# Kernel tuning notes

Hardware: AMD Instinct MI355X
Metric: run time of the kernel (lower is better)

Reference implementation:

```python
import jax, jax.numpy as jnp
import numpy as np

B, S, H, W = 64, 32, 40, 64
SENS, UNITS, MOTOR, NA = 1283, 48, 4, 2
UNFOLDS = 6  # ncps LTC default ode_unfolds
EPS = 1e-8


def setup_inputs() -> dict:
    key = jax.random.key(0)
    ks = iter(jax.random.split(key, 40))
    u = lambda sh, lo, hi: jax.random.uniform(next(ks), sh, jnp.float32, lo, hi)
    inp = {}
    inp["depth_image"] = jax.random.uniform(next(ks), (B, S, H, W), jnp.float32)
    inp["relative_position"] = jax.random.normal(next(ks), (B, S, 3), jnp.float32)
    # CNN params (conv k3 s2 p1 + ReLU) x3: 1->32->64->32
    def cw(o, i):
        return jax.random.normal(next(ks), (o, i, 3, 3), jnp.float32) / np.sqrt(i * 9.0)
    inp["w1"], inp["b1"] = cw(32, 1), jnp.zeros((32,), jnp.float32)
    inp["w2"], inp["b2"] = cw(64, 32), jnp.zeros((64,), jnp.float32)
    inp["w3"], inp["b3"] = cw(32, 64), jnp.zeros((32,), jnp.float32)
    # LTC cell params (ncps init ranges)
    inp["input_w"] = jnp.ones((SENS,), jnp.float32)
    inp["input_b"] = jnp.zeros((SENS,), jnp.float32)
    inp["sens_w"] = u((SENS, UNITS), 0.001, 1.0)
    inp["sens_mu"] = u((SENS, UNITS), 0.3, 0.8)
    inp["sens_sigma"] = u((SENS, UNITS), 3.0, 8.0)
    inp["sens_erev"] = jnp.sign(jax.random.normal(next(ks), (SENS, UNITS)))
    inp["rec_w"] = u((UNITS, UNITS), 0.001, 1.0)
    inp["rec_mu"] = u((UNITS, UNITS), 0.3, 0.8)
    inp["rec_sigma"] = u((UNITS, UNITS), 3.0, 8.0)
    inp["rec_erev"] = jnp.sign(jax.random.normal(next(ks), (UNITS, UNITS)))
    inp["gleak"] = u((UNITS,), 0.001, 1.0)
    inp["vleak"] = u((UNITS,), -0.2, 0.2)
    inp["cm"] = u((UNITS,), 0.4, 0.6)
    inp["out_w"] = jnp.ones((MOTOR,), jnp.float32)
    inp["out_b"] = jnp.zeros((MOTOR,), jnp.float32)
    inp["head_w"] = jax.random.normal(next(ks), (MOTOR, NA), jnp.float32) * 0.5
    inp["head_b"] = jnp.zeros((NA,), jnp.float32)
    inp["sens_mask"] = (jax.random.uniform(next(ks), (SENS, UNITS)) < 0.3).astype(jnp.int32)
    inp["rec_mask"] = (jax.random.uniform(next(ks), (UNITS, UNITS)) < 0.3).astype(jnp.int32)
    return inp


def _conv(x, w, b):
    y = jax.lax.conv_general_dilated(x, w, (2, 2), [(1, 1), (1, 1)],
                                     dimension_numbers=("NCHW", "OIHW", "NCHW"))
    return jax.nn.relu(y + b[None, :, None, None])


def reference(depth_image, relative_position, w1, b1, w2, b2, w3, b3,
              input_w, input_b, sens_w, sens_mu, sens_sigma, sens_erev,
              rec_w, rec_mu, rec_sigma, rec_erev, gleak, vleak, cm,
              out_w, out_b, head_w, head_b, sens_mask, rec_mask):
    b, s = depth_image.shape[:2]
    x = depth_image.reshape(b * s, 1, H, W)
    x = _conv(_conv(_conv(x, w1, b1), w2, b2), w3, b3)  # [b*s,32,5,8]
    feat = x.reshape(b, s, -1)  # [b,s,1280]
    seq = jnp.concatenate([feat, relative_position.reshape(b, s, -1)], axis=2)  # [b,s,1283]

    sp = jax.nn.softplus
    smask = sens_mask.astype(seq.dtype)
    rmask = rec_mask.astype(seq.dtype)
    cm_t = sp(cm) * UNFOLDS          # cm / (elapsed_time / ode_unfolds), dt=1
    gl = sp(gleak)
    sw_pos = sp(sens_w) * smask
    rw_pos = sp(rec_w) * rmask

    def step(v, xt):  # xt: [b, SENS]
        I = xt * input_w + input_b
        # sensory synapse activations: [b, SENS, UNITS]
        sa = sw_pos * jax.nn.sigmoid(sens_sigma * (I[:, :, None] - sens_mu))
        w_num_s = (sa * sens_erev).sum(1)  # [b, UNITS]
        w_den_s = sa.sum(1)
        def unfold(v, _):
            ra = rw_pos * jax.nn.sigmoid(rec_sigma * (v[:, :, None] - rec_mu))
            num = cm_t * v + gl * vleak + (ra * rec_erev).sum(1) + w_num_s
            den = cm_t + gl + ra.sum(1) + w_den_s
            return num / (den + EPS), None
        v, _ = jax.lax.scan(unfold, v, None, length=UNFOLDS)
        y = v[:, :MOTOR] * out_w + out_b  # motor neuron readout
        return v, y

    v0 = jnp.zeros((b, UNITS), seq.dtype)
    _, ys = jax.lax.scan(step, v0, jnp.swapaxes(seq, 0, 1))  # [s, b, MOTOR]
    pooled = ys.mean(0)  # mean over seq dim
    return jnp.tanh(pooled @ head_w + head_b)  # [b, NA] action mean
```

## Files before the change

### kernel.cpp

```cpp
#include <hip/hip_runtime.h>
#include <hip/hip_bf16.h>


typedef __attribute__((ext_vector_type(8))) short bshort8;
typedef __attribute__((ext_vector_type(4))) float f32x4;

constexpr long OFF_SEQ  = 0;
constexpr long OFF_SP4  = 2627584;
constexpr long OFF_RP4  = 2873920;
constexpr long OFF_CM   = 2886208;
constexpr long OFF_W2B  = 2886400;
constexpr long OFF_W3B  = 2898688;
constexpr long OFF_PART = 2907904;

__device__ __forceinline__ float sp_(float x) {
    return fmaxf(x, 0.f) + log1pf(expf(-fabsf(x)));
}

__device__ __forceinline__ float qxor1_(float x) {
    return __int_as_float(__builtin_amdgcn_mov_dpp(__float_as_int(x), 0xB1, 0xF, 0xF, true));
}
__device__ __forceinline__ float qxor2_(float x) {
    return __int_as_float(__builtin_amdgcn_mov_dpp(__float_as_int(x), 0x4E, 0xF, 0xF, true));
}

__global__ void prep_kernel(const float* __restrict__ sens_w, const float* __restrict__ sens_mu,
                            const float* __restrict__ sens_sigma, const float* __restrict__ sens_erev,
                            const int* __restrict__ sens_mask,
                            const float* __restrict__ rec_w, const float* __restrict__ rec_mu,
                            const float* __restrict__ rec_sigma, const float* __restrict__ rec_erev,
                            const int* __restrict__ rec_mask,
                            const float* __restrict__ gleak, const float* __restrict__ vleak,
                            const float* __restrict__ cm,
                            const float* __restrict__ w2, const float* __restrict__ w3,
                            float* __restrict__ ws) {
    const float L2E = 1.4426950408889634f;
    int i = blockIdx.x * 256 + threadIdx.x;
    if (i < 61584) {
        float m  = sens_mask[i] ? 1.f : 0.f;
        float sw = sp_(sens_w[i]) * m;
        float sg = sens_sigma[i], mu = sens_mu[i];
        ((float4*)(ws + OFF_SP4))[i] =
            make_float4(-sg * L2E, sg * mu * L2E, sw * sens_erev[i], sw);
    } else if (i < 64656) {
        int q = i - 61584;
        int j = q >> 6, u = q & 63;
        float4 v = make_float4(0.f, 0.f, 0.f, 0.f);
        if (u < 48) {
            int idx = j * 48 + u;
            float m  = rec_mask[idx] ? 1.f : 0.f;
            float sw = sp_(rec_w[idx]) * m;
            float sg = rec_sigma[idx], mu = rec_mu[idx];
            v = make_float4(-sg * L2E, sg * mu * L2E, sw * rec_erev[idx], sw);
        }
        ((float4*)(ws + OFF_RP4))[q] = v;
    } else if (i < 64704) {
        int u = i - 64656;
        float g = sp_(gleak[u]);
        ws[OFF_CM + u]       = sp_(cm[u]) * 6.f;
        ws[OFF_CM + 64 + u]  = g;
        ws[OFF_CM + 128 + u] = g * vleak[u];
    } else if (i < 89280) {
        int n = i - 64704;
        int j = n & 7, l = (n >> 3) & 63, t2 = n >> 9;
        int wv = t2 & 3;
        int r  = t2 >> 2;
        int xp = r & 1, hk = r >> 1;
        int ky = hk % 3, h = hk / 3;
        int oc = wv * 16 + (l & 15);
        int kgB = l >> 4;
        int icl = (kgB & 1) * 8 + j;
        int ic = h * 16 + icl;
        int kx = 2 * xp + (kgB >> 1);
        float val = (kx == 3) ? 0.f : w2[((oc * 32 + ic) * 3 + ky) * 3 + kx];
        ((__hip_bfloat16*)(ws + OFF_W2B))[n] = __float2bfloat16(val);
    } else if (i < 107712) {
        int n = i - 89280;
        int j = n & 7, l = (n >> 3) & 63, t3 = n >> 9;
        int h = t3 & 1, u2 = t3 >> 1;
        int nt = u2 / 9, p = u2 % 9;
        int ky = p / 3, kx = p % 3;
        int oc = nt * 16 + (l & 15);
        int ic = h * 32 + (l >> 4) * 8 + j;
        ((__hip_bfloat16*)(ws + OFF_W3B))[n] =
            __float2bfloat16(w3[((oc * 64 + ic) * 3 + ky) * 3 + kx]);
    }
}

#define IMGB 0
#define C1H  5424
#define A2E  0
#define A2O  12672
#define SMB  28272

__global__ __launch_bounds__(256, 4) void cnn_kernel(
    const float* __restrict__ depth, const float* __restrict__ relpos,
    const float* __restrict__ w1, const float* __restrict__ b1,
    const float* __restrict__ b2, const float* __restrict__ b3,
    const __hip_bfloat16* __restrict__ w2b, const __hip_bfloat16* __restrict__ w3b,
    float* __restrict__ seq) {
    __shared__ __align__(16) char smraw[SMB];
    const int t = threadIdx.x;
    const int img = blockIdx.x;
    const int l = t & 63;
    const int wvu = __builtin_amdgcn_readfirstlane(t >> 6);
    const int m = l & 15, kg = l >> 4;

    for (int i = t; i < 7068; i += 256) ((uint*)smraw)[i] = 0u;
    __syncthreads();
    for (int i = t; i < 1280; i += 256) {
        int pos = 2 * i;
        int h = pos >> 6, w = pos & 63;
        float2 d = *(const float2*)(depth + (long)img * 2560 + pos);
        __hip_bfloat162 pk = __float22bfloat162_rn(d);
        *(__hip_bfloat162*)(smraw + IMGB + ((h + 1) * 66 + (w + 2)) * 2) = pk;
    }
    __syncthreads();

    const __hip_bfloat16* imgp = (const __hip_bfloat16*)(smraw + IMGB);
    f32x4 acc[10];
    {
        float bias = b2[wvu * 16 + m];
#pragma unroll
        for (int mt = 0; mt < 10; ++mt) acc[mt] = (f32x4){bias, bias, bias, bias};
    }

#pragma unroll 1
    for (int h = 0; h < 2; ++h) {
        const int ocb = h * 16 + wvu * 4;
        float wv4[4][9], bv4[4];
#pragma unroll
        for (int j = 0; j < 4; ++j) {
            bv4[j] = b1[ocb + j];
#pragma unroll
            for (int k = 0; k < 9; ++k) wv4[j][k] = w1[(ocb + j) * 9 + k];
        }
#pragma unroll 1
        for (int i = 0; i < 10; ++i) {
            int p = l + (i << 6);
            int y1 = p >> 5, x1 = p & 31;
            float xin[9];
#pragma unroll
            for (int ky = 0; ky < 3; ++ky)
#pragma unroll
                for (int kx = 0; kx < 3; ++kx)
                    xin[ky * 3 + kx] = __bfloat162float(imgp[(2 * y1 + ky) * 66 + 2 * x1 + kx + 1]);
            float o[4];
#pragma unroll
            for (int j = 0; j < 4; ++j) {
                float a = bv4[j];
#pragma unroll
                for (int k = 0; k < 9; ++k) a = fmaf(wv4[j][k], xin[k], a);
                o[j] = fmaxf(a, 0.f);
            }
            char* cb = smraw + C1H + (((y1 + 1) * 34) + (x1 + 1)) * 32 + wvu * 8;
            *(__hip_bfloat162*)cb       = __float22bfloat162_rn(make_float2(o[0], o[1]));
            *(__hip_bfloat162*)(cb + 4) = __float22bfloat162_rn(make_float2(o[2], o[3]));
        }
        bshort8 Bh[6];
#pragma unroll
        for (int f = 0; f < 6; ++f)
            Bh[f] = *(const bshort8*)(w2b + (((h * 6 + f) * 4 + wvu) * 64 + l) * 8);
        __syncthreads();
#pragma unroll
        for (int ky = 0; ky < 3; ++ky) {
#pragma unroll
            for (int xp = 0; xp < 2; ++xp) {
                bshort8 Bp = Bh[ky * 2 + xp];
                const char* base = smraw + C1H + (ky * 34 + 2 * m + 2 * xp + (kg >> 1)) * 32 + (kg & 1) * 16;
#pragma unroll
                for (int mt = 0; mt < 10; ++mt) {
                    bshort8 A = *(const bshort8*)(base + mt * 2176);
                    acc[mt] = __builtin_amdgcn_mfma_f32_16x16x32_bf16(A, Bp, acc[mt], 0, 0, 0);
                }
            }
        }
        __syncthreads();
    }

    for (int i = t; i < 6336; i += 256) ((uint*)smraw)[i] = 0u;
    __syncthreads();
    {
        int oc = wvu * 16 + m;
        int q = oc >> 3, sub = oc & 7;
#pragma unroll
        for (int mt = 0; mt < 10; ++mt) {
            int row = mt + 1;
#pragma unroll
            for (int reg = 0; reg < 4; ++reg) {
                int x2 = kg * 4 + reg;
                int odd = x2 & 1;
                int xi = odd ? ((x2 + 1) >> 1) : (x2 >> 1);
                char* ab = smraw + (odd ? A2O : A2E);
                float v = fmaxf(acc[mt][reg], 0.f);
                *(__hip_bfloat16*)(ab + (((q * 11 + row) * 9 + xi) * 8 + sub) * 2) = __float2bfloat16(v);
            }
        }
    }
    __syncthreads();

    {
        const int nt = wvu & 1;
        const bool two = wvu < 2;
        f32x4 c3a = (f32x4){0.f, 0.f, 0.f, 0.f};
        f32x4 c3b = (f32x4){0.f, 0.f, 0.f, 0.f};
        const int xb = m & 7, yb = m >> 3;
#pragma unroll
        for (int p = 0; p < 9; ++p) {
            int ky = p / 3, kx = p % 3;
            const char* arr = smraw + ((kx == 1) ? A2E : A2O);
            int xi3 = xb + (kx == 2);
#pragma unroll
            for (int h = 0; h < 2; ++h) {
                bshort8 B = *(const bshort8*)(w3b + (((nt * 9 + p) * 2 + h) * 64 + l) * 8);
                int q = h * 4 + kg;
                const char* base = arr + ((q * 11 + 2 * yb + ky) * 9 + xi3) * 16;
                if (two) {
                    bshort8 A0 = *(const bshort8*)(base);
                    c3a = __builtin_amdgcn_mfma_f32_16x16x32_bf16(A0, B, c3a, 0, 0, 0);
                    bshort8 A2 = *(const bshort8*)(base + 1152);
                    c3b = __builtin_amdgcn_mfma_f32_16x16x32_bf16(A2, B, c3b, 0, 0, 0);
                } else {
                    bshort8 A1 = *(const bshort8*)(base + 576);
                    c3a = __builtin_amdgcn_mfma_f32_16x16x32_bf16(A1, B, c3a, 0, 0, 0);
                }
            }
        }
        __syncthreads();
        float* sb = (float*)smraw;
        int oc = nt * 16 + m;
        float bv = b3[oc];
        int ob40 = oc * 40;
        if (two) {
#pragma unroll
            for (int reg = 0; reg < 4; ++reg) {
                sb[ob40 + kg * 4 + reg] = fmaxf(c3a[reg] + bv, 0.f);
                int px2 = 32 + kg * 4 + reg;
                if (px2 < 40) sb[ob40 + px2] = fmaxf(c3b[reg] + bv, 0.f);
            }
        } else {
#pragma unroll
            for (int reg = 0; reg < 4; ++reg)
                sb[ob40 + 16 + kg * 4 + reg] = fmaxf(c3a[reg] + bv, 0.f);
        }
        __syncthreads();
        for (int i = t; i < 1283; i += 256)
            seq[(long)img * 1283 + i] = (i < 1280) ? sb[i] : relpos[img * 3 + (i - 1280)];
    }
}

__global__ __launch_bounds__(768) void sensory_kernel(
    const float* __restrict__ sp, const float* __restrict__ seq,
    const float* __restrict__ iw, const float* __restrict__ ibias,
    float2* __restrict__ part) {
    const float4* P4 = (const float4*)sp;
    __shared__ __align__(16) char sbuf[49152];
    float*  IT  = (float*)sbuf;
    float2* red = (float2*)sbuf;
    const int t = threadIdx.x;
    const int pb = blockIdx.x * 8;

    for (int p = 0; p < 8; ++p)
        for (int k = t; k < 1283; k += 768)
            IT[k * 8 + p] = fmaf(seq[(long)(pb + p) * 1283 + k], iw[k], ibias[k]);
    __syncthreads();

    const int u = t % 48, kg = t / 48;
    float2 acc[8];
#pragma unroll
    for (int p = 0; p < 8; ++p) acc[p] = make_float2(0.f, 0.f);

#pragma unroll 2
    for (int i = 0; i < 81; ++i) {
        int k = kg + 16 * i;
        if (k < 1283) {
            float4 pv = P4[k * 48 + u];
            float4 Ia = *(const float4*)&IT[k * 8];
            float4 Ib = *(const float4*)&IT[k * 8 + 4];
            float r0 = __builtin_amdgcn_rcpf(1.f + __builtin_amdgcn_exp2f(fmaf(pv.x, Ia.x, pv.y)));
            float r1 = __builtin_amdgcn_rcpf(1.f + __builtin_amdgcn_exp2f(fmaf(pv.x, Ia.y, pv.y)));
            float r2 = __builtin_amdgcn_rcpf(1.f + __builtin_amdgcn_exp2f(fmaf(pv.x, Ia.z, pv.y)));
            float r3 = __builtin_amdgcn_rcpf(1.f + __builtin_amdgcn_exp2f(fmaf(pv.x, Ia.w, pv.y)));
            float r4 = __builtin_amdgcn_rcpf(1.f + __builtin_amdgcn_exp2f(fmaf(pv.x, Ib.x, pv.y)));
            float r5 = __builtin_amdgcn_rcpf(1.f + __builtin_amdgcn_exp2f(fmaf(pv.x, Ib.y, pv.y)));
            float r6 = __builtin_amdgcn_rcpf(1.f + __builtin_amdgcn_exp2f(fmaf(pv.x, Ib.z, pv.y)));
            float r7 = __builtin_amdgcn_rcpf(1.f + __builtin_amdgcn_exp2f(fmaf(pv.x, Ib.w, pv.y)));
            acc[0].x = fmaf(pv.z, r0, acc[0].x); acc[0].y = fmaf(pv.w, r0, acc[0].y);
            acc[1].x = fmaf(pv.z, r1, acc[1].x); acc[1].y = fmaf(pv.w, r1, acc[1].y);
            acc[2].x = fmaf(pv.z, r2, acc[2].x); acc[2].y = fmaf(pv.w, r2, acc[2].y);
            acc[3].x = fmaf(pv.z, r3, acc[3].x); acc[3].y = fmaf(pv.w, r3, acc[3].y);
            acc[4].x = fmaf(pv.z, r4, acc[4].x); acc[4].y = fmaf(pv.w, r4, acc[4].y);
            acc[5].x = fmaf(pv.z, r5, acc[5].x); acc[5].y = fmaf(pv.w, r5, acc[5].y);
            acc[6].x = fmaf(pv.z, r6, acc[6].x); acc[6].y = fmaf(pv.w, r6, acc[6].y);
            acc[7].x = fmaf(pv.z, r7, acc[7].x); acc[7].y = fmaf(pv.w, r7, acc[7].y);
        }
    }
    __syncthreads();
#pragma unroll
    for (int p = 0; p < 8; ++p) red[(kg * 8 + p) * 48 + u] = acc[p];
    __syncthreads();
    if (t < 384) {
        int p = t / 48, uu = t - p * 48;
        float sn = 0.f, sd = 0.f;
#pragma unroll
        for (int g = 0; g < 16; ++g) {
            float2 rr = red[(g * 8 + p) * 48 + uu];
            sn += rr.x; sd += rr.y;
        }
        part[(long)(pb + p) * 48 + uu] = make_float2(sn, sd);
    }
}

__global__ __launch_bounds__(192, 1) void recurrent_kernel(
    const float* __restrict__ rp, const float* __restrict__ cmglv,
    const float2* __restrict__ part,
    const float* __restrict__ out_w, const float* __restrict__ out_b,
    const float* __restrict__ head_w, const float* __restrict__ head_b,
    float* __restrict__ outp) {
    __shared__ float2 WL[1536];
    __shared__ float  LV[2][64];
    __shared__ float  ym[4];
    const int t  = threadIdx.x;
    const int b  = blockIdx.x;
    const int u  = t >> 2;
    const int jq = t & 3;

    const float4* RP4 = (const float4*)rp;
    float4 P[12];
#pragma unroll
    for (int r = 0; r < 12; ++r) P[r] = RP4[(jq * 12 + r) * 64 + u];
#pragma unroll
    for (int r = 0; r < 12; ++r) {
        asm volatile("" : "+v"(P[r].x), "+v"(P[r].y), "+v"(P[r].z), "+v"(P[r].w));
    }

    for (int i = t; i < 1536; i += 192) WL[i] = part[(long)b * 1536 + i];
    if (t < 64) { LV[0][t] = 0.f; LV[1][t] = 0.f; }

    const float cmt = cmglv[u], gl = cmglv[64 + u], glv = cmglv[128 + u];
    const float cg  = cmt + gl + 1e-8f;
    float ow = 0.f, ob = 0.f;
    const bool lead = (jq == 0) && (u < 4);
    if (lead) { ow = out_w[u]; ob = out_b[u]; }
    __syncthreads();

    float vn = 0.f, yacc = 0.f;
    int buf = 0;
#pragma unroll 1
    for (int s = 0; s < 32; ++s) {
        float2 wnd = WL[s * 48 + u];
        const float basen = glv + wnd.x;
        const float based = cg + wnd.y;
#pragma unroll
        for (int unf = 0; unf < 6; ++unf) {
            const float4* lv4 = (const float4*)&LV[buf][jq * 12];
            float4 V0 = lv4[0], V1 = lv4[1], V2 = lv4[2];
            float va[12] = {V0.x, V0.y, V0.z, V0.w, V1.x, V1.y, V1.z, V1.w,
                            V2.x, V2.y, V2.z, V2.w};
            float pn = 0.f, pd = 0.f;
#pragma unroll
            for (int r = 0; r < 12; ++r) {
                float rr = __builtin_amdgcn_rcpf(
                    1.f + __builtin_amdgcn_exp2f(fmaf(P[r].x, va[r], P[r].y)));
                pn = fmaf(P[r].z, rr, pn);
                pd = fmaf(P[r].w, rr, pd);
            }
            pn += qxor1_(pn); pd += qxor1_(pd);
            pn += qxor2_(pn); pd += qxor2_(pd);
            float num = fmaf(cmt, vn, basen) + pn;
            float den = based + pd;
            float r0 = __builtin_amdgcn_rcpf(den);
            r0 = r0 * fmaf(-den, r0, 2.f);
            vn = num * r0;
            if (jq == 0) LV[buf ^ 1][u] = vn;
            __syncthreads();
            buf ^= 1;
        }
        if (lead) yacc = fmaf(vn, ow, yacc) + ob;
    }
    if (lead) ym[u] = yacc;
    __syncthreads();
    if (t < 2) {
        const float inv = 1.f / 32.f;
        float o = fmaf(ym[0] * inv, head_w[t],
                  fmaf(ym[1] * inv, head_w[2 + t],
                  fmaf(ym[2] * inv, head_w[4 + t],
                  fmaf(ym[3] * inv, head_w[6 + t], head_b[t]))));
        outp[b * 2 + t] = tanhf(o);
    }
}

extern "C" void kernel_launch(void* const* d_in, const int* in_sizes, int n_in,
                              void* d_out, int out_size, void* d_ws, size_t ws_size,
                              hipStream_t stream) {
    const float* depth      = (const float*)d_in[0];
    const float* relpos     = (const float*)d_in[1];
    const float* w1         = (const float*)d_in[2];
    const float* b1         = (const float*)d_in[3];
    const float* w2         = (const float*)d_in[4];
    const float* b2         = (const float*)d_in[5];
    const float* w3         = (const float*)d_in[6];
    const float* b3         = (const float*)d_in[7];
    const float* iw         = (const float*)d_in[8];
    const float* ibias      = (const float*)d_in[9];
    const float* sens_w     = (const float*)d_in[10];
    const float* sens_mu    = (const float*)d_in[11];
    const float* sens_sigma = (const float*)d_in[12];
    const float* sens_erev  = (const float*)d_in[13];
    const float* rec_w      = (const float*)d_in[14];
    const float* rec_mu     = (const float*)d_in[15];
    const float* rec_sigma  = (const float*)d_in[16];
    const float* rec_erev   = (const float*)d_in[17];
    const float* gleak      = (const float*)d_in[18];
    const float* vleak      = (const float*)d_in[19];
    const float* cm         = (const float*)d_in[20];
    const float* out_w      = (const float*)d_in[21];
    const float* out_b      = (const float*)d_in[22];
    const float* head_w     = (const float*)d_in[23];
    const float* head_b     = (const float*)d_in[24];
    const int*   sens_mask  = (const int*)d_in[25];
    const int*   rec_mask   = (const int*)d_in[26];

    float* ws  = (float*)d_ws;
    float* out = (float*)d_out;

    prep_kernel<<<477, 256, 0, stream>>>(sens_w, sens_mu, sens_sigma, sens_erev, sens_mask,
                                         rec_w, rec_mu, rec_sigma, rec_erev, rec_mask,
                                         gleak, vleak, cm, w2, w3, ws);
    cnn_kernel<<<2048, 256, 0, stream>>>(depth, relpos, w1, b1, b2, b3,
                                         (const __hip_bfloat16*)(ws + OFF_W2B),
                                         (const __hip_bfloat16*)(ws + OFF_W3B),
                                         ws + OFF_SEQ);
    sensory_kernel<<<256, 768, 0, stream>>>(ws + OFF_SP4, ws + OFF_SEQ, iw, ibias,
                                            (float2*)(ws + OFF_PART));
    recurrent_kernel<<<64, 192, 0, stream>>>(ws + OFF_RP4, ws + OFF_CM,
                                             (const float2*)(ws + OFF_PART),
                                             out_w, out_b, head_w, head_b, out);
}
```

Baseline: 274.7 us.

## Process two batch elements per block in recurrent kernel

Each recurrent block now advances two independent batch sequences together, interleaving their sigmoid and reduction chains so the two dependency chains can hide each other's latency, and shares the barriers between them. The grid is halved from 64 to 32 blocks. The cost is fewer blocks on a GPU with many idle compute units, and more registers and LDS per block.

Measured after the change: 311.1 us. 13.2% more time.

```diff
diff --git a/kernel.cpp b/kernel.cpp
--- a/kernel.cpp
+++ b/kernel.cpp
@@ -317,11 +317,11 @@
     const float* __restrict__ out_w, const float* __restrict__ out_b,
     const float* __restrict__ head_w, const float* __restrict__ head_b,
     float* __restrict__ outp) {
-    __shared__ float2 WL[1536];
-    __shared__ float  LV[2][64];
-    __shared__ float  ym[4];
+    __shared__ float2 WL[2][1536];
+    __shared__ float  LV[2][2][64];
+    __shared__ float  ym[2][4];
     const int t  = threadIdx.x;
-    const int b  = blockIdx.x;
+    const int bA = blockIdx.x * 2;
     const int u  = t >> 2;
     const int jq = t & 3;
 
@@ -334,8 +334,11 @@
         asm volatile("" : "+v"(P[r].x), "+v"(P[r].y), "+v"(P[r].z), "+v"(P[r].w));
     }
 
-    for (int i = t; i < 1536; i += 192) WL[i] = part[(long)b * 1536 + i];
-    if (t < 64) { LV[0][t] = 0.f; LV[1][t] = 0.f; }
+    for (int i = t; i < 3072; i += 192) {
+        int lb = i / 1536, li = i - lb * 1536;
+        WL[lb][li] = part[(long)(bA + lb) * 1536 + li];
+    }
+    if (t < 64) { LV[0][0][t] = 0.f; LV[0][1][t] = 0.f; LV[1][0][t] = 0.f; LV[1][1][t] = 0.f; }
 
     const float cmt = cmglv[u], gl = cmglv[64 + u], glv = cmglv[128 + u];
     const float cg  = cmt + gl + 1e-8f;
@@ -344,49 +347,64 @@
     if (lead) { ow = out_w[u]; ob = out_b[u]; }
     __syncthreads();
 
-    float vn = 0.f, yacc = 0.f;
+    float vnA = 0.f, vnB = 0.f, yaccA = 0.f, yaccB = 0.f;
     int buf = 0;
 #pragma unroll 1
     for (int s = 0; s < 32; ++s) {
-        float2 wnd = WL[s * 48 + u];
-        const float basen = glv + wnd.x;
-        const float based = cg + wnd.y;
+        float2 wA = WL[0][s * 48 + u];
+        float2 wB = WL[1][s * 48 + u];
+        const float basenA = glv + wA.x, basedA = cg + wA.y;
+        const float basenB = glv + wB.x, basedB = cg + wB.y;
 #pragma unroll
         for (int unf = 0; unf < 6; ++unf) {
-            const float4* lv4 = (const float4*)&LV[buf][jq * 12];
-            float4 V0 = lv4[0], V1 = lv4[1], V2 = lv4[2];
-            float va[12] = {V0.x, V0.y, V0.z, V0.w, V1.x, V1.y, V1.z, V1.w,
-                            V2.x, V2.y, V2.z, V2.w};
-            float pn = 0.f, pd = 0.f;
+            const float4* lvA = (const float4*)&LV[0][buf][jq * 12];
+            const float4* lvB = (const float4*)&LV[1][buf][jq * 12];
+            float4 A0 = lvA[0], A1 = lvA[1], A2 = lvA[2];
+            float4 B0 = lvB[0], B1 = lvB[1], B2 = lvB[2];
+            float vaA[12] = {A0.x, A0.y, A0.z, A0.w, A1.x, A1.y, A1.z, A1.w,
+                             A2.x, A2.y, A2.z, A2.w};
+            float vaB[12] = {B0.x, B0.y, B0.z, B0.w, B1.x, B1.y, B1.z, B1.w,
+                             B2.x, B2.y, B2.z, B2.w};
+            float pnA = 0.f, pdA = 0.f, pnB = 0.f, pdB = 0.f;
 #pragma unroll
             for (int r = 0; r < 12; ++r) {
-                float rr = __builtin_amdgcn_rcpf(
-                    1.f + __builtin_amdgcn_exp2f(fmaf(P[r].x, va[r], P[r].y)));
-                pn = fmaf(P[r].z, rr, pn);
-                pd = fmaf(P[r].w, rr, pd);
-            }
-            pn += qxor1_(pn); pd += qxor1_(pd);
-            pn += qxor2_(pn); pd += qxor2_(pd);
-            float num = fmaf(cmt, vn, basen) + pn;
-            float den = based + pd;
-            float r0 = __builtin_amdgcn_rcpf(den);
-            r0 = r0 * fmaf(-den, r0, 2.f);
-            vn = num * r0;
-            if (jq == 0) LV[buf ^ 1][u] = vn;
+                float rA = __builtin_amdgcn_rcpf(
+                    1.f + __builtin_amdgcn_exp2f(fmaf(P[r].x, vaA[r], P[r].y)));
+                float rB = __builtin_amdgcn_rcpf(
+                    1.f + __builtin_amdgcn_exp2f(fmaf(P[r].x, vaB[r], P[r].y)));
+                pnA = fmaf(P[r].z, rA, pnA); pdA = fmaf(P[r].w, rA, pdA);
+                pnB = fmaf(P[r].z, rB, pnB); pdB = fmaf(P[r].w, rB, pdB);
+            }
+            pnA += qxor1_(pnA); pdA += qxor1_(pdA);
+            pnB += qxor1_(pnB); pdB += qxor1_(pdB);
+            pnA += qxor2_(pnA); pdA += qxor2_(pdA);
+            pnB += qxor2_(pnB); pdB += qxor2_(pdB);
+            float numA = fmaf(cmt, vnA, basenA) + pnA;
+            float denA = basedA + pdA;
+            float numB = fmaf(cmt, vnB, basenB) + pnB;
+            float denB = basedB + pdB;
+            float rA0 = __builtin_amdgcn_rcpf(denA);
+            rA0 = rA0 * fmaf(-denA, rA0, 2.f);
+            float rB0 = __builtin_amdgcn_rcpf(denB);
+            rB0 = rB0 * fmaf(-denB, rB0, 2.f);
+            vnA = numA * rA0;
+            vnB = numB * rB0;
+            if (jq == 0) { LV[0][buf ^ 1][u] = vnA; LV[1][buf ^ 1][u] = vnB; }
             __syncthreads();
             buf ^= 1;
         }
-        if (lead) yacc = fmaf(vn, ow, yacc) + ob;
-    }
-    if (lead) ym[u] = yacc;
-    __syncthreads();
-    if (t < 2) {
+        if (lead) { yaccA = fmaf(vnA, ow, yaccA) + ob; yaccB = fmaf(vnB, ow, yaccB) + ob; }
+    }
+    if (lead) { ym[0][u] = yaccA; ym[1][u] = yaccB; }
+    __syncthreads();
+    if (t < 4) {
+        int lb = t >> 1, g = t & 1;
         const float inv = 1.f / 32.f;
-        float o = fmaf(ym[0] * inv, head_w[t],
-                  fmaf(ym[1] * inv, head_w[2 + t],
-                  fmaf(ym[2] * inv, head_w[4 + t],
-                  fmaf(ym[3] * inv, head_w[6 + t], head_b[t]))));
-        outp[b * 2 + t] = tanhf(o);
+        float o = fmaf(ym[lb][0] * inv, head_w[g],
+                  fmaf(ym[lb][1] * inv, head_w[2 + g],
+                  fmaf(ym[lb][2] * inv, head_w[4 + g],
+                  fmaf(ym[lb][3] * inv, head_w[6 + g], head_b[g]))));
+        outp[(bA + lb) * 2 + g] = tanhf(o);
     }
 }
 
@@ -433,7 +451,7 @@
                                          ws + OFF_SEQ);
     sensory_kernel<<<256, 768, 0, stream>>>(ws + OFF_SP4, ws + OFF_SEQ, iw, ibias,
                                             (float2*)(ws + OFF_PART));
-    recurrent_kernel<<<64, 192, 0, stream>>>(ws + OFF_RP4, ws + OFF_CM,
+    recurrent_kernel<<<32, 192, 0, stream>>>(ws + OFF_RP4, ws + OFF_CM,
                                              (const float2*)(ws + OFF_PART),
                                              out_w, out_b, head_w, head_b, out);
 }
```

## Compact sparse sensory synapses per unit and iterate only over masked entries

Applied to the files above, without the earlier changes.

A new kernel builds, for each of the 48 units, a compacted list of the sensory synapses whose mask is set. It stores the precomputed parameters and source indices, capped at 480 entries and zero-padded. The sensory kernel now loops over 30 compacted entries per thread group instead of all 1283 inputs, cutting the exp/rcp work that previously ran on masked-out synapses. The input activations are transposed in shared memory so they can be gathered by index, which may cause LDS bank conflicts. The fixed capacity silently drops synapses if a unit ever has more than 480 connections.

Result: faster. 261.4 us (-4.9%).

```diff
diff --git a/kernel.cpp b/kernel.cpp
--- a/kernel.cpp
+++ b/kernel.cpp
@@ -13,6 +13,8 @@
 constexpr long OFF_W3B  = 2898688;
 constexpr long OFF_PART = 2907904;
 
+constexpr int SCAP = 480;
+
 __device__ __forceinline__ float sp_(float x) {
     return fmaxf(x, 0.f) + log1pf(expf(-fabsf(x)));
 }
@@ -24,10 +26,7 @@
     return __int_as_float(__builtin_amdgcn_mov_dpp(__float_as_int(x), 0x4E, 0xF, 0xF, true));
 }
 
-__global__ void prep_kernel(const float* __restrict__ sens_w, const float* __restrict__ sens_mu,
-                            const float* __restrict__ sens_sigma, const float* __restrict__ sens_erev,
-                            const int* __restrict__ sens_mask,
-                            const float* __restrict__ rec_w, const float* __restrict__ rec_mu,
+__global__ void prep_kernel(const float* __restrict__ rec_w, const float* __restrict__ rec_mu,
                             const float* __restrict__ rec_sigma, const float* __restrict__ rec_erev,
                             const int* __restrict__ rec_mask,
                             const float* __restrict__ gleak, const float* __restrict__ vleak,
@@ -35,14 +34,8 @@
                             const float* __restrict__ w2, const float* __restrict__ w3,
                             float* __restrict__ ws) {
     const float L2E = 1.4426950408889634f;
-    int i = blockIdx.x * 256 + threadIdx.x;
-    if (i < 61584) {
-        float m  = sens_mask[i] ? 1.f : 0.f;
-        float sw = sp_(sens_w[i]) * m;
-        float sg = sens_sigma[i], mu = sens_mu[i];
-        ((float4*)(ws + OFF_SP4))[i] =
-            make_float4(-sg * L2E, sg * mu * L2E, sw * sens_erev[i], sw);
-    } else if (i < 64656) {
+    int i = blockIdx.x * 256 + threadIdx.x + 61584;
+    if (i < 64656) {
         int q = i - 61584;
         int j = q >> 6, u = q & 63;
         float4 v = make_float4(0.f, 0.f, 0.f, 0.f);
@@ -87,6 +80,54 @@
     }
 }
 
+__global__ __launch_bounds__(256) void sens_compact_kernel(
+    const float* __restrict__ sens_w, const float* __restrict__ sens_mu,
+    const float* __restrict__ sens_sigma, const float* __restrict__ sens_erev,
+    const int* __restrict__ sens_mask, float* __restrict__ ws) {
+    const float L2E = 1.4426950408889634f;
+    float4* cp4 = (float4*)(ws + OFF_SP4);
+    int* kix = (int*)(ws + OFF_SP4 + 98304);
+    int* nnz = (int*)(ws + OFF_SP4 + 122880);
+    const int u = blockIdx.x;
+    const int t = threadIdx.x;
+    const int w = t >> 6, lane = t & 63;
+    __shared__ int wcnt[4];
+    __shared__ int basetot;
+    if (t == 0) basetot = 0;
+    __syncthreads();
+#pragma unroll 1
+    for (int c = 0; c < 6; ++c) {
+        int k = c * 256 + t;
+        bool m = (k < 1283) && (sens_mask[k * 48 + u] != 0);
+        unsigned long long bal = __ballot(m);
+        int prefix = __popcll(bal & ((1ULL << lane) - 1ULL));
+        if (lane == 0) wcnt[w] = __popcll(bal);
+        __syncthreads();
+        int wbase = basetot;
+        for (int ww = 0; ww < 4; ++ww) if (ww < w) wbase += wcnt[ww];
+        if (m) {
+            int pos = wbase + prefix;
+            if (pos < SCAP) {
+                int idx = k * 48 + u;
+                float sw = sp_(sens_w[idx]);
+                float sg = sens_sigma[idx], mu = sens_mu[idx];
+                cp4[pos * 48 + u] = make_float4(-sg * L2E, sg * mu * L2E,
+                                                sw * sens_erev[idx], sw);
+                kix[pos * 48 + u] = k;
+            }
+        }
+        __syncthreads();
+        if (t == 0) basetot += wcnt[0] + wcnt[1] + wcnt[2] + wcnt[3];
+        __syncthreads();
+    }
+    int cnt = min(basetot, SCAP);
+    for (int e = cnt + t; e < SCAP; e += 256) {
+        cp4[e * 48 + u] = make_float4(0.f, 0.f, 0.f, 0.f);
+        kix[e * 48 + u] = 0;
+    }
+    if (t == 0) nnz[u] = cnt;
+}
+
 #define IMGB 0
 #define C1H  5424
 #define A2E  0
@@ -253,7 +294,8 @@
     const float* __restrict__ sp, const float* __restrict__ seq,
     const float* __restrict__ iw, const float* __restrict__ ibias,
     float2* __restrict__ part) {
-    const float4* P4 = (const float4*)sp;
+    const float4* CP4 = (const float4*)sp;
+    const int* KIX = (const int*)(sp + 98304);
     __shared__ __align__(16) char sbuf[49152];
     float*  IT  = (float*)sbuf;
     float2* red = (float2*)sbuf;
@@ -262,7 +304,7 @@
 
     for (int p = 0; p < 8; ++p)
         for (int k = t; k < 1283; k += 768)
-            IT[k * 8 + p] = fmaf(seq[(long)(pb + p) * 1283 + k], iw[k], ibias[k]);
+            IT[p * 1288 + k] = fmaf(seq[(long)(pb + p) * 1283 + k], iw[k], ibias[k]);
     __syncthreads();
 
     const int u = t % 48, kg = t / 48;
@@ -271,29 +313,27 @@
     for (int p = 0; p < 8; ++p) acc[p] = make_float2(0.f, 0.f);
 
 #pragma unroll 2
-    for (int i = 0; i < 81; ++i) {
-        int k = kg + 16 * i;
-        if (k < 1283) {
-            float4 pv = P4[k * 48 + u];
-            float4 Ia = *(const float4*)&IT[k * 8];
-            float4 Ib = *(const float4*)&IT[k * 8 + 4];
-            float r0 = __builtin_amdgcn_rcpf(1.f + __builtin_amdgcn_exp2f(fmaf(pv.x, Ia.x, pv.y)));
-            float r1 = __builtin_amdgcn_rcpf(1.f + __builtin_amdgcn_exp2f(fmaf(pv.x, Ia.y, pv.y)));
-            float r2 = __builtin_amdgcn_rcpf(1.f + __builtin_amdgcn_exp2f(fmaf(pv.x, Ia.z, pv.y)));
-            float r3 = __builtin_amdgcn_rcpf(1.f + __builtin_amdgcn_exp2f(fmaf(pv.x, Ia.w, pv.y)));
-            float r4 = __builtin_amdgcn_rcpf(1.f + __builtin_amdgcn_exp2f(fmaf(pv.x, Ib.x, pv.y)));
-            float r5 = __builtin_amdgcn_rcpf(1.f + __builtin_amdgcn_exp2f(fmaf(pv.x, Ib.y, pv.y)));
-            float r6 = __builtin_amdgcn_rcpf(1.f + __builtin_amdgcn_exp2f(fmaf(pv.x, Ib.z, pv.y)));
-            float r7 = __builtin_amdgcn_rcpf(1.f + __builtin_amdgcn_exp2f(fmaf(pv.x, Ib.w, pv.y)));
-            acc[0].x = fmaf(pv.z, r0, acc[0].x); acc[0].y = fmaf(pv.w, r0, acc[0].y);
-            acc[1].x = fmaf(pv.z, r1, acc[1].x); acc[1].y = fmaf(pv.w, r1, acc[1].y);
-            acc[2].x = fmaf(pv.z, r2, acc[2].x); acc[2].y = fmaf(pv.w, r2, acc[2].y);
-            acc[3].x = fmaf(pv.z, r3, acc[3].x); acc[3].y = fmaf(pv.w, r3, acc[3].y);
-            acc[4].x = fmaf(pv.z, r4, acc[4].x); acc[4].y = fmaf(pv.w, r4, acc[4].y);
-            acc[5].x = fmaf(pv.z, r5, acc[5].x); acc[5].y = fmaf(pv.w, r5, acc[5].y);
-            acc[6].x = fmaf(pv.z, r6, acc[6].x); acc[6].y = fmaf(pv.w, r6, acc[6].y);
-            acc[7].x = fmaf(pv.z, r7, acc[7].x); acc[7].y = fmaf(pv.w, r7, acc[7].y);
-        }
+    for (int i = 0; i < 30; ++i) {
+        int e = kg + 16 * i;
+        float4 pv = CP4[e * 48 + u];
+        int k = KIX[e * 48 + u];
+        const float* itk = IT + k;
+        float r0 = __builtin_amdgcn_rcpf(1.f + __builtin_amdgcn_exp2f(fmaf(pv.x, itk[0 * 1288], pv.y)));
+        float r1 = __builtin_amdgcn_rcpf(1.f + __builtin_amdgcn_exp2f(fmaf(pv.x, itk[1 * 1288], pv.y)));
+        float r2 = __builtin_amdgcn_rcpf(1.f + __builtin_amdgcn_exp2f(fmaf(pv.x, itk[2 * 1288], pv.y)));
+        float r3 = __builtin_amdgcn_rcpf(1.f + __builtin_amdgcn_exp2f(fmaf(pv.x, itk[3 * 1288], pv.y)));
+        float r4 = __builtin_amdgcn_rcpf(1.f + __builtin_amdgcn_exp2f(fmaf(pv.x, itk[4 * 1288], pv.y)));
+        float r5 = __builtin_amdgcn_rcpf(1.f + __builtin_amdgcn_exp2f(fmaf(pv.x, itk[5 * 1288], pv.y)));
+        float r6 = __builtin_amdgcn_rcpf(1.f + __builtin_amdgcn_exp2f(fmaf(pv.x, itk[6 * 1288], pv.y)));
+        float r7 = __builtin_amdgcn_rcpf(1.f + __builtin_amdgcn_exp2f(fmaf(pv.x, itk[7 * 1288], pv.y)));
+        acc[0].x = fmaf(pv.z, r0, acc[0].x); acc[0].y = fmaf(pv.w, r0, acc[0].y);
+        acc[1].x = fmaf(pv.z, r1, acc[1].x); acc[1].y = fmaf(pv.w, r1, acc[1].y);
+        acc[2].x = fmaf(pv.z, r2, acc[2].x); acc[2].y = fmaf(pv.w, r2, acc[2].y);
+        acc[3].x = fmaf(pv.z, r3, acc[3].x); acc[3].y = fmaf(pv.w, r3, acc[3].y);
+        acc[4].x = fmaf(pv.z, r4, acc[4].x); acc[4].y = fmaf(pv.w, r4, acc[4].y);
+        acc[5].x = fmaf(pv.z, r5, acc[5].x); acc[5].y = fmaf(pv.w, r5, acc[5].y);
+        acc[6].x = fmaf(pv.z, r6, acc[6].x); acc[6].y = fmaf(pv.w, r6, acc[6].y);
+        acc[7].x = fmaf(pv.z, r7, acc[7].x); acc[7].y = fmaf(pv.w, r7, acc[7].y);
     }
     __syncthreads();
 #pragma unroll
@@ -424,9 +464,10 @@
     float* ws  = (float*)d_ws;
     float* out = (float*)d_out;
 
-    prep_kernel<<<477, 256, 0, stream>>>(sens_w, sens_mu, sens_sigma, sens_erev, sens_mask,
-                                         rec_w, rec_mu, rec_sigma, rec_erev, rec_mask,
+    prep_kernel<<<181, 256, 0, stream>>>(rec_w, rec_mu, rec_sigma, rec_erev, rec_mask,
                                          gleak, vleak, cm, w2, w3, ws);
+    sens_compact_kernel<<<48, 256, 0, stream>>>(sens_w, sens_mu, sens_sigma, sens_erev,
+                                                sens_mask, ws);
     cnn_kernel<<<2048, 256, 0, stream>>>(depth, relpos, w1, b1, b2, b3,
                                          (const __hip_bfloat16*)(ws + OFF_W2B),
                                          (const __hip_bfloat16*)(ws + OFF_W3B),
```
